# Kernel optimization log

Hardware: AMD Instinct MI355X
Metric: run time of the kernel (lower is better)

The kernel has to match this reference:

```python
import jax, jax.numpy as jnp
import numpy as np

B, T, D = 256, 1024, 128
L, O = 16, 256

_ACTS = [jnp.tanh, jax.nn.relu, jax.nn.sigmoid, lambda z: z] * 4


def setup_inputs() -> dict:
    key = jax.random.key(0)
    k = jax.random.split(key, 5)
    return {
        "x": jax.random.normal(k[0], (B, T, D), dtype=jnp.float32),
        # Dense(1) kernels for the L sub-layers, stacked: [L, D]; biases [L]
        "sub_W": jax.random.uniform(k[1], (L, D), dtype=jnp.float32, minval=-0.05, maxval=0.05),
        "sub_b": jnp.zeros((L,), dtype=jnp.float32),
        "agg_W": jax.random.uniform(k[2], (L, O), dtype=jnp.float32, minval=-0.05, maxval=0.05),
        "R": jax.random.uniform(k[3], (O, O), dtype=jnp.float32, minval=-0.05, maxval=0.05),
    }


def reference(x, sub_W, sub_b, agg_W, R):
    # All Dense(1) sub-layers are state-independent -> precompute for all t.
    # pre: [B, T, L] = per-sub-layer scalar projection of each timestep input
    pre = jnp.einsum("btd,ld->btl", x, sub_W) + sub_b
    act = jnp.stack([_ACTS[i](pre[..., i]) for i in range(L)], axis=-1)  # [B,T,L]
    # aggregation matmul, also state-independent: [B, T, O]
    agg = jnp.einsum("btl,lo->bto", act, agg_W)

    # recurrence: state = linear(state); state = agg_t + state @ R
    def step(state, a_t):
        new_state = a_t + state @ R
        return new_state, new_state

    init = jnp.zeros((x.shape[0], R.shape[0]), dtype=x.dtype)
    _, ys = jax.lax.scan(step, init, jnp.swapaxes(agg, 0, 1))  # ys: [T,B,O]
    return jnp.swapaxes(ys, 0, 1)  # [B, T, O] (return_sequences=True)
```

## Files before the change

### kernel.cpp

```cpp
#include <hip/hip_runtime.h>
#include <math.h>

#define BB 256
#define TT 1024
#define DD 128
#define LL 16
#define OO 256
#define TILE 16
#define DPAD 132
#define CPAD 20


template<int CTRL>
__device__ __forceinline__ float dpp_mov(float v) {
    return __builtin_bit_cast(float,
        __builtin_amdgcn_update_dpp(0, __builtin_bit_cast(int, v),
                                    CTRL, 0xF, 0xF, true));
}
__device__ __forceinline__ float swz_xor4(float v) {
    return __builtin_bit_cast(float,
        __builtin_amdgcn_ds_swizzle(__builtin_bit_cast(int, v), 0x101F));
}
__device__ __forceinline__ void bar_lds() {
    asm volatile("s_waitcnt lgkmcnt(0)" ::: "memory");
    __builtin_amdgcn_s_barrier();
}

__global__ __launch_bounds__(512, 2)
void srkan_fused(const float* __restrict__ x,
                 const float* __restrict__ subW,
                 const float* __restrict__ subb,
                 const float* __restrict__ aggW,
                 const float* __restrict__ R,
                 float* __restrict__ y)
{
    const int b    = blockIdx.x;
    const int tid  = threadIdx.x;
    const int lane = tid & 63;
    const int w    = tid >> 6;
    const int og   = lane >> 4;
    const int ic   = lane & 15;

    __shared__ float sW[LL][DPAD];
    __shared__ float xs[TILE][DPAD];
    __shared__ float acts[TILE][LL];
    __shared__ float aggt[TILE][OO];
    __shared__ float aggWt[OO][CPAD];
    __shared__ float sbuf[2][16][CPAD];
    __shared__ float bias[LL];

    {
        const int idx = tid * 4;
        const int l = idx >> 7, d = idx & 127;
        *(float4*)&sW[l][d] = *(const float4*)&subW[idx];
    }
    if (tid < LL) bias[tid] = subb[tid];
#pragma unroll
    for (int h = 0; h < 2; ++h) {
        const int idx = (tid + h * 512) * 4;
        const int l = idx >> 8, o0 = idx & 255;
        float4 v = *(const float4*)&aggW[idx];
        aggWt[o0 + 0][l] = v.x; aggWt[o0 + 1][l] = v.y;
        aggWt[o0 + 2][l] = v.z; aggWt[o0 + 3][l] = v.w;
    }
    for (int i = tid; i < 2 * 16 * CPAD; i += 512)
        ((float*)sbuf)[i] = 0.f;

    const int o_base = w * 32 + og * 8;
    float r[8][16];
    {
        const float* Rp = R + (size_t)(ic * 16) * OO + o_base;
#pragma unroll
        for (int j = 0; j < 16; ++j) {
            float4 lo = *(const float4*)(Rp + (size_t)j * OO);
            float4 hi = *(const float4*)(Rp + (size_t)j * OO + 4);
            r[0][j] = lo.x; r[1][j] = lo.y; r[2][j] = lo.z; r[3][j] = lo.w;
            r[4][j] = hi.x; r[5][j] = hi.y; r[6][j] = hi.z; r[7][j] = hi.w;
        }
    }

    const int v_ic   = 4 * (ic & 1) + 2 * ((ic >> 1) & 1) + ((ic >> 3) & 1);
    const bool writer = (ic & 4) == 0;
    const int o_w    = o_base + v_ic;
    const int c_w    = o_w >> 4, e_w = o_w & 15;

    bar_lds();

    const float* xb = x + (size_t)b * TT * DD;
    float*       yb = y + (size_t)b * TT * OO;

    const int xp_tt = tid >> 5, xp_d = (tid * 4) & 127;
    float4 xpre = *(const float4*)&xb[tid * 4];

#pragma unroll 1
    for (int t0 = 0; t0 < TT; t0 += TILE) {
        if (t0) {
#pragma unroll
            for (int h = 0; h < 2; ++h) {
                const int idx = h * 2048 + tid * 4;
                const int tt = idx >> 8, o = idx & 255;
                float4 v = *(const float4*)&aggt[tt][o];
                *(float4*)&yb[(size_t)(t0 - TILE + tt) * OO + o] = v;
            }
        }
        *(float4*)&xs[xp_tt][xp_d] = xpre;
        bar_lds();

        {
            const int dot = tid >> 1, q = tid & 1;
            const int tt = dot >> 4, l = dot & 15;
            const float4* xv = (const float4*)&xs[tt][q * 64];
            const float4* wv = (const float4*)&sW[l][q * 64];
            float p0 = 0.f, p1 = 0.f, p2 = 0.f, p3 = 0.f;
#pragma unroll
            for (int j = 0; j < 16; ++j) {
                float4 a = xv[j], vv = wv[j];
                p0 += a.x * vv.x; p1 += a.y * vv.y;
                p2 += a.z * vv.z; p3 += a.w * vv.w;
            }
            float p = (p0 + p1) + (p2 + p3);
            p += dpp_mov<0xB1>(p);
            if (q == 0) {
                p += bias[l];
                float v;
                switch (l & 3) {
                    case 0:  v = tanhf(p); break;
                    case 1:  v = fmaxf(p, 0.f); break;
                    case 2:  v = 1.f / (1.f + expf(-p)); break;
                    default: v = p; break;
                }
                acts[tt][l] = v;
            }
        }
        bar_lds();

        {
            const int g = tid >> 8;
            const int o = tid & 255;
            const float4* aw = (const float4*)&aggWt[o][0];
            float4 w0 = aw[0], w1 = aw[1], w2 = aw[2], w3 = aw[3];
#pragma unroll
            for (int kk = 0; kk < 8; ++kk) {
                const int tt = g * 8 + kk;
                const float4* av = (const float4*)&acts[tt][0];
                float4 a0 = av[0], a1 = av[1], a2 = av[2], a3 = av[3];
                float s0 = a0.x * w0.x + a0.y * w0.y + a0.z * w0.z + a0.w * w0.w;
                float s1 = a1.x * w1.x + a1.y * w1.y + a1.z * w1.z + a1.w * w1.w;
                float s2 = a2.x * w2.x + a2.y * w2.y + a2.z * w2.z + a2.w * w2.w;
                float s3 = a3.x * w3.x + a3.y * w3.y + a3.z * w3.z + a3.w * w3.w;
                aggt[tt][o] = (s0 + s1) + (s2 + s3);
            }
        }
        if (t0 + TILE < TT)
            xpre = *(const float4*)&xb[(size_t)(t0 + TILE) * DD + tid * 4];
        bar_lds();

#pragma unroll 2
        for (int k = 0; k < TILE; ++k) {
            const int cur = k & 1;
            const float4* s4 = (const float4*)&sbuf[cur][ic][0];
            float4 s0 = s4[0], s1 = s4[1], s2 = s4[2], s3 = s4[3];
            float p[8];
#pragma unroll
            for (int v = 0; v < 8; ++v) p[v] = 0.f;
#pragma unroll
            for (int jb = 0; jb < 4; ++jb) {
                const float4 sv = (jb == 0) ? s0 : (jb == 1) ? s1
                                 : (jb == 2) ? s2 : s3;
#pragma unroll
                for (int e = 0; e < 4; ++e) {
                    const float sj = (e == 0) ? sv.x : (e == 1) ? sv.y
                                    : (e == 2) ? sv.z : sv.w;
#pragma unroll
                    for (int v = 0; v < 8; ++v)
                        p[v] += sj * r[v][jb * 4 + e];
                }
            }
            float q1a[4];
            {
                const bool e = (ic & 1) == 0;
#pragma unroll
                for (int m = 0; m < 4; ++m) {
                    float a  = e ? p[m] : p[4 + m];
                    float bb = e ? p[4 + m] : p[m];
                    q1a[m] = a + dpp_mov<0xB1>(bb);
                }
            }
            float q2a[2];
            {
                const bool e = (ic & 2) == 0;
#pragma unroll
                for (int m = 0; m < 2; ++m) {
                    float a  = e ? q1a[m] : q1a[2 + m];
                    float bb = e ? q1a[2 + m] : q1a[m];
                    q2a[m] = a + dpp_mov<0x4E>(bb);
                }
            }
            float u;
            {
                const bool e = (ic & 8) == 0;
                float a  = e ? q2a[0] : q2a[1];
                float bb = e ? q2a[1] : q2a[0];
                u = a + dpp_mov<0x128>(bb);
            }
            u += swz_xor4(u);
            if (writer) {
                const float ns = u + aggt[k][o_w];
                sbuf[cur ^ 1][c_w][e_w] = ns;
                aggt[k][o_w] = ns;
            }
            bar_lds();
        }
    }

#pragma unroll
    for (int h = 0; h < 2; ++h) {
        const int idx = h * 2048 + tid * 4;
        const int tt = idx >> 8, o = idx & 255;
        float4 v = *(const float4*)&aggt[tt][o];
        *(float4*)&yb[(size_t)(TT - TILE + tt) * OO + o] = v;
    }
}

extern "C" void kernel_launch(void* const* d_in, const int* in_sizes, int n_in,
                              void* d_out, int out_size, void* d_ws, size_t ws_size,
                              hipStream_t stream) {
    const float* x    = (const float*)d_in[0];
    const float* subW = (const float*)d_in[1];
    const float* subb = (const float*)d_in[2];
    const float* aggW = (const float*)d_in[3];
    const float* R    = (const float*)d_in[4];
    float* yp = (float*)d_out;

    srkan_fused<<<BB, 512, 0, stream>>>(x, subW, subb, aggW, R, yp);
}
```

Baseline: 898.4 us.

## Use packed FP32 FMA with pre-permuted R registers and simplified DPP reduction

Recurrence weights are stored as two-float vectors, pre-permuted per lane at load time so the butterfly reduction needs no per-step selects. The inner matvec then uses packed FMA, which can issue as v_pk_fma_f32. The aggregation and projection stages also use packed FMA, with aggW held in registers instead of a transposed LDS copy. Scheduling fences are added around barriers. The aim is to shorten the serial per-timestep critical path, at some cost in register pressure.

```diff
diff --git a/kernel.cpp b/kernel.cpp
--- a/kernel.cpp
+++ b/kernel.cpp
@@ -8,8 +8,11 @@
 #define OO 256
 #define TILE 16
 #define DPAD 132
+#define APAD 20
 #define CPAD 20
 
+
+typedef float v2f __attribute__((ext_vector_type(2)));
 
 template<int CTRL>
 __device__ __forceinline__ float dpp_mov(float v) {
@@ -24,6 +27,12 @@
 __device__ __forceinline__ void bar_lds() {
     asm volatile("s_waitcnt lgkmcnt(0)" ::: "memory");
     __builtin_amdgcn_s_barrier();
+}
+__device__ __forceinline__ void sched_fence() {
+    __builtin_amdgcn_sched_barrier(0);
+}
+__device__ __forceinline__ v2f mk2(float a, float b) {
+    v2f r; r.x = a; r.y = b; return r;
 }
 
 __global__ __launch_bounds__(512, 2)
@@ -43,9 +52,8 @@
 
     __shared__ float sW[LL][DPAD];
     __shared__ float xs[TILE][DPAD];
-    __shared__ float acts[TILE][LL];
+    __shared__ float acts[TILE][APAD];
     __shared__ float aggt[TILE][OO];
-    __shared__ float aggWt[OO][CPAD];
     __shared__ float sbuf[2][16][CPAD];
     __shared__ float bias[LL];
 
@@ -55,34 +63,42 @@
         *(float4*)&sW[l][d] = *(const float4*)&subW[idx];
     }
     if (tid < LL) bias[tid] = subb[tid];
-#pragma unroll
-    for (int h = 0; h < 2; ++h) {
-        const int idx = (tid + h * 512) * 4;
-        const int l = idx >> 8, o0 = idx & 255;
-        float4 v = *(const float4*)&aggW[idx];
-        aggWt[o0 + 0][l] = v.x; aggWt[o0 + 1][l] = v.y;
-        aggWt[o0 + 2][l] = v.z; aggWt[o0 + 3][l] = v.w;
-    }
     for (int i = tid; i < 2 * 16 * CPAD; i += 512)
         ((float*)sbuf)[i] = 0.f;
 
+    const int o_d = tid & 255;
+    v2f aw2[8];
+#pragma unroll
+    for (int h = 0; h < 8; ++h)
+        aw2[h] = mk2(aggW[(2 * h) * OO + o_d], aggW[(2 * h + 1) * OO + o_d]);
+
     const int o_base = w * 32 + og * 8;
-    float r[8][16];
+    const int f0 = (ic >> 3) & 1, f1 = (ic >> 1) & 1, f2 = ic & 1;
+    v2f r2[4][16];
     {
         const float* Rp = R + (size_t)(ic * 16) * OO + o_base;
 #pragma unroll
         for (int j = 0; j < 16; ++j) {
             float4 lo = *(const float4*)(Rp + (size_t)j * OO);
             float4 hi = *(const float4*)(Rp + (size_t)j * OO + 4);
-            r[0][j] = lo.x; r[1][j] = lo.y; r[2][j] = lo.z; r[3][j] = lo.w;
-            r[4][j] = hi.x; r[5][j] = hi.y; r[6][j] = hi.z; r[7][j] = hi.w;
-        }
-    }
-
-    const int v_ic   = 4 * (ic & 1) + 2 * ((ic >> 1) & 1) + ((ic >> 3) & 1);
+            float l0 = f1 ? lo.z : lo.x, l1 = f1 ? lo.w : lo.y;
+            float l2 = f1 ? lo.x : lo.z, l3 = f1 ? lo.y : lo.w;
+            float h0 = f1 ? hi.z : hi.x, h1 = f1 ? hi.w : hi.y;
+            float h2 = f1 ? hi.x : hi.z, h3 = f1 ? hi.y : hi.w;
+            float m0 = f0 ? l1 : l0, m1 = f0 ? l0 : l1;
+            float m2 = f0 ? l3 : l2, m3 = f0 ? l2 : l3;
+            float n0 = f0 ? h1 : h0, n1 = f0 ? h0 : h1;
+            float n2 = f0 ? h3 : h2, n3 = f0 ? h2 : h3;
+            r2[0][j] = f2 ? mk2(n0, m0) : mk2(m0, n0);
+            r2[1][j] = f2 ? mk2(n1, m1) : mk2(m1, n1);
+            r2[2][j] = f2 ? mk2(n2, m2) : mk2(m2, n2);
+            r2[3][j] = f2 ? mk2(n3, m3) : mk2(m3, n3);
+        }
+    }
+
     const bool writer = (ic & 4) == 0;
-    const int o_w    = o_base + v_ic;
-    const int c_w    = o_w >> 4, e_w = o_w & 15;
+    const int o_w = o_base + 4 * f2 + 2 * f1 + f0;
+    const int c_w = o_w >> 4, e_w = o_w & 15;
 
     bar_lds();
 
@@ -105,20 +121,21 @@
         }
         *(float4*)&xs[xp_tt][xp_d] = xpre;
         bar_lds();
+        sched_fence();
 
         {
             const int dot = tid >> 1, q = tid & 1;
             const int tt = dot >> 4, l = dot & 15;
             const float4* xv = (const float4*)&xs[tt][q * 64];
             const float4* wv = (const float4*)&sW[l][q * 64];
-            float p0 = 0.f, p1 = 0.f, p2 = 0.f, p3 = 0.f;
-#pragma unroll
+            v2f acc0 = mk2(0.f, 0.f), acc1 = mk2(0.f, 0.f);
+#pragma unroll 4
             for (int j = 0; j < 16; ++j) {
                 float4 a = xv[j], vv = wv[j];
-                p0 += a.x * vv.x; p1 += a.y * vv.y;
-                p2 += a.z * vv.z; p3 += a.w * vv.w;
-            }
-            float p = (p0 + p1) + (p2 + p3);
+                acc0 = __builtin_elementwise_fma(mk2(a.x, a.y), mk2(vv.x, vv.y), acc0);
+                acc1 = __builtin_elementwise_fma(mk2(a.z, a.w), mk2(vv.z, vv.w), acc1);
+            }
+            float p = (acc0.x + acc0.y) + (acc1.x + acc1.y);
             p += dpp_mov<0xB1>(p);
             if (q == 0) {
                 p += bias[l];
@@ -132,27 +149,30 @@
                 acts[tt][l] = v;
             }
         }
+        sched_fence();
         bar_lds();
 
         {
             const int g = tid >> 8;
-            const int o = tid & 255;
-            const float4* aw = (const float4*)&aggWt[o][0];
-            float4 w0 = aw[0], w1 = aw[1], w2 = aw[2], w3 = aw[3];
 #pragma unroll
             for (int kk = 0; kk < 8; ++kk) {
                 const int tt = g * 8 + kk;
                 const float4* av = (const float4*)&acts[tt][0];
                 float4 a0 = av[0], a1 = av[1], a2 = av[2], a3 = av[3];
-                float s0 = a0.x * w0.x + a0.y * w0.y + a0.z * w0.z + a0.w * w0.w;
-                float s1 = a1.x * w1.x + a1.y * w1.y + a1.z * w1.z + a1.w * w1.w;
-                float s2 = a2.x * w2.x + a2.y * w2.y + a2.z * w2.z + a2.w * w2.w;
-                float s3 = a3.x * w3.x + a3.y * w3.y + a3.z * w3.z + a3.w * w3.w;
-                aggt[tt][o] = (s0 + s1) + (s2 + s3);
+                v2f acc = mk2(a0.x, a0.y) * aw2[0];
+                acc = __builtin_elementwise_fma(mk2(a0.z, a0.w), aw2[1], acc);
+                acc = __builtin_elementwise_fma(mk2(a1.x, a1.y), aw2[2], acc);
+                acc = __builtin_elementwise_fma(mk2(a1.z, a1.w), aw2[3], acc);
+                acc = __builtin_elementwise_fma(mk2(a2.x, a2.y), aw2[4], acc);
+                acc = __builtin_elementwise_fma(mk2(a2.z, a2.w), aw2[5], acc);
+                acc = __builtin_elementwise_fma(mk2(a3.x, a3.y), aw2[6], acc);
+                acc = __builtin_elementwise_fma(mk2(a3.z, a3.w), aw2[7], acc);
+                aggt[tt][o_d] = acc.x + acc.y;
             }
         }
         if (t0 + TILE < TT)
             xpre = *(const float4*)&xb[(size_t)(t0 + TILE) * DD + tid * 4];
+        sched_fence();
         bar_lds();
 
 #pragma unroll 2
@@ -160,49 +180,35 @@
             const int cur = k & 1;
             const float4* s4 = (const float4*)&sbuf[cur][ic][0];
             float4 s0 = s4[0], s1 = s4[1], s2 = s4[2], s3 = s4[3];
-            float p[8];
-#pragma unroll
-            for (int v = 0; v < 8; ++v) p[v] = 0.f;
+            v2f p2[4];
+            {
+                const v2f sc = mk2(s0.x, s0.x);
+                p2[0] = sc * r2[0][0]; p2[1] = sc * r2[1][0];
+                p2[2] = sc * r2[2][0]; p2[3] = sc * r2[3][0];
+            }
 #pragma unroll
             for (int jb = 0; jb < 4; ++jb) {
-                const float4 sv = (jb == 0) ? s0 : (jb == 1) ? s1
-                                 : (jb == 2) ? s2 : s3;
+                const float4 sv = jb == 0 ? s0 : jb == 1 ? s1 : jb == 2 ? s2 : s3;
 #pragma unroll
                 for (int e = 0; e < 4; ++e) {
-                    const float sj = (e == 0) ? sv.x : (e == 1) ? sv.y
-                                    : (e == 2) ? sv.z : sv.w;
-#pragma unroll
-                    for (int v = 0; v < 8; ++v)
-                        p[v] += sj * r[v][jb * 4 + e];
+                    if (jb == 0 && e == 0) continue;
+                    const float sj = e == 0 ? sv.x : e == 1 ? sv.y
+                                   : e == 2 ? sv.z : sv.w;
+                    const v2f sc = mk2(sj, sj);
+                    const int j = jb * 4 + e;
+                    p2[0] = __builtin_elementwise_fma(sc, r2[0][j], p2[0]);
+                    p2[1] = __builtin_elementwise_fma(sc, r2[1][j], p2[1]);
+                    p2[2] = __builtin_elementwise_fma(sc, r2[2][j], p2[2]);
+                    p2[3] = __builtin_elementwise_fma(sc, r2[3][j], p2[3]);
                 }
             }
-            float q1a[4];
-            {
-                const bool e = (ic & 1) == 0;
-#pragma unroll
-                for (int m = 0; m < 4; ++m) {
-                    float a  = e ? p[m] : p[4 + m];
-                    float bb = e ? p[4 + m] : p[m];
-                    q1a[m] = a + dpp_mov<0xB1>(bb);
-                }
-            }
-            float q2a[2];
-            {
-                const bool e = (ic & 2) == 0;
-#pragma unroll
-                for (int m = 0; m < 2; ++m) {
-                    float a  = e ? q1a[m] : q1a[2 + m];
-                    float bb = e ? q1a[2 + m] : q1a[m];
-                    q2a[m] = a + dpp_mov<0x4E>(bb);
-                }
-            }
-            float u;
-            {
-                const bool e = (ic & 8) == 0;
-                float a  = e ? q2a[0] : q2a[1];
-                float bb = e ? q2a[1] : q2a[0];
-                u = a + dpp_mov<0x128>(bb);
-            }
+            float q0 = p2[0].x + dpp_mov<0xB1>(p2[0].y);
+            float q1 = p2[1].x + dpp_mov<0xB1>(p2[1].y);
+            float q2 = p2[2].x + dpp_mov<0xB1>(p2[2].y);
+            float q3 = p2[3].x + dpp_mov<0xB1>(p2[3].y);
+            float u0 = q0 + dpp_mov<0x4E>(q2);
+            float u1 = q1 + dpp_mov<0x4E>(q3);
+            float u  = u0 + dpp_mov<0x128>(u1);
             u += swz_xor4(u);
             if (writer) {
                 const float ns = u + aggt[k][o_w];
```

Measured after the change: 851.5 us. -5.2%, faster.
